# Performance work log

Hardware: AMD Instinct MI355X
Metric: run time of the kernel (lower is better)

The kernel has to match this reference:

```python
import jax, jax.numpy as jnp
import numpy as np

N_NODES = 500000
N_EDGES = 8000000
IN_DIM = 128
H1, H2, OUT = 32, 16, 2


def gcn_conv(x, W, b, src, dst, n):
    # PyG GCNConv: linear transform, add self-loops, symmetric norm, scatter-add, +bias
    x = x @ W                                   # [N, out]
    loop = jnp.arange(n, dtype=src.dtype)
    s = jnp.concatenate([src, loop])            # [E+N]
    d = jnp.concatenate([dst, loop])            # [E+N]
    deg = jax.ops.segment_sum(jnp.ones_like(d, dtype=x.dtype), d, num_segments=n)
    dinv = jnp.where(deg > 0, jax.lax.rsqrt(deg), 0.0)
    norm = dinv[s] * dinv[d]                    # [E+N]
    msg = x[s] * norm[:, None]                  # [E+N, out] gather
    out = jax.ops.segment_sum(msg, d, num_segments=n)  # scatter-add
    return out + b


def setup_inputs() -> dict:
    key = jax.random.key(0)
    ks = jax.random.split(key, 8)
    x = jax.random.normal(ks[0], (N_NODES, IN_DIM), dtype=jnp.float32)
    edge_index = jax.random.randint(ks[1], (2, N_EDGES), 0, N_NODES, dtype=jnp.int64)
    def glorot(k, fan_in, fan_out):
        lim = float(np.sqrt(6.0 / (fan_in + fan_out)))
        return jax.random.uniform(k, (fan_in, fan_out), jnp.float32, -lim, lim)
    return {
        "x": x,
        "edge_index": edge_index,
        "W1": glorot(ks[2], IN_DIM, H1),
        "b1": jnp.zeros((H1,), jnp.float32),
        "W2": glorot(ks[3], H1, H2),
        "b2": jnp.zeros((H2,), jnp.float32),
        "Wfc": glorot(ks[4], H2, OUT),
        "bfc": jnp.zeros((OUT,), jnp.float32),
    }


def reference(x, edge_index, W1, b1, W2, b2, Wfc, bfc):
    src, dst = edge_index[0], edge_index[1]
    h = jax.nn.relu(gcn_conv(x, W1, b1, src, dst, x.shape[0]))
    h = jax.nn.relu(gcn_conv(h, W2, b2, src, dst, x.shape[0]))
    logits = h @ Wfc + bfc
    return jax.nn.log_softmax(logits, axis=1)
```

## Files before the change

kernel.cpp:

```cpp
#include <hip/hip_runtime.h>

#define N_NODES 500000
#define N_EDGES 8000000
#define IN_DIM 128
#define H1 32
#define H2 16
#define NFINE 1954
#define NCOARSE 62
#define CAPA 200
#define CAPB 340

static __device__ __forceinline__ float bf2f(unsigned short u) {
    return __uint_as_float(((unsigned int)u) << 16);
}
static __device__ __forceinline__ unsigned short f2bf(float f) {
    unsigned int u = __float_as_uint(f);
    unsigned int r = (u + 0x7fffu + ((u >> 16) & 1u)) >> 16;
    return (unsigned short)r;
}
static __device__ __forceinline__ unsigned pack2bf(float a, float b) {
    return (unsigned)f2bf(a) | ((unsigned)f2bf(b) << 16);
}
static __device__ __forceinline__ float ldf(const void* p, int i, bool isf32) {
    return isf32 ? ((const float*)p)[i] : bf2f(((const unsigned short*)p)[i]);
}

__global__ __launch_bounds__(64) void k_sniff(const unsigned int* __restrict__ x,
                                              int* __restrict__ flag) {
    int bad = 0;
    for (int i = threadIdx.x; i < 1024; i += 64) {
        float v = __uint_as_float((x[i] & 0xffffu) << 16);
        if (!(fabsf(v) < 1e6f)) bad = 1;
    }
    unsigned long long m = __ballot(bad);
    if (threadIdx.x == 0) *flag = (m != 0ull) ? 1 : 0;
}

__global__ __launch_bounds__(256) void k_bhist(const int* __restrict__ dst,
                                               int* __restrict__ fhist) {
    __shared__ int h[2048];
    int tid = threadIdx.x;
    for (int i = tid; i < 2048; i += 256) h[i] = 0;
    __syncthreads();
    int i = blockIdx.x * 256 + tid;
    int stride = gridDim.x * 256;
    for (int e = i; e < N_EDGES; e += stride) {
        unsigned d = (unsigned)dst[e];
        if (d < N_NODES) atomicAdd(&h[d >> 8], 1);
    }
    __syncthreads();
    for (int i2 = tid; i2 < 2048; i2 += 256)
        if (h[i2]) atomicAdd(&fhist[i2], h[i2]);
}

__global__ __launch_bounds__(256) void k_scanf(const int* __restrict__ fhist,
                                               int* __restrict__ fbase,
                                               int* __restrict__ bcur,
                                               int* __restrict__ acur) {
    __shared__ int tmp[256];
    __shared__ int s_run;
    int tid = threadIdx.x;
    if (tid == 0) s_run = 0;
    __syncthreads();
    for (int base = 0; base < 2048; base += 256) {
        int i = base + tid;
        int v = (i < NFINE) ? fhist[i] : 0;
        int val = v;
        tmp[tid] = val;
        __syncthreads();
        for (int o = 1; o < 256; o <<= 1) {
            int t = (tid >= o) ? tmp[tid - o] : 0;
            __syncthreads();
            val += t;
            tmp[tid] = val;
            __syncthreads();
        }
        int run = s_run;
        if (i < NFINE) {
            int ex = run + val - v;
            fbase[i] = ex;
            bcur[i] = ex;
            if ((i & 31) == 0) acur[i >> 5] = ex;
        }
        __syncthreads();
        if (tid == 255) s_run = run + val;
        __syncthreads();
    }
    if (tid == 0) fbase[NFINE] = s_run;
}

__global__ __launch_bounds__(256) void k_scatA(const int* __restrict__ src,
                                               const int* __restrict__ dst,
                                               int* __restrict__ acur,
                                               unsigned* __restrict__ ebufA) {
    __shared__ unsigned stage[NCOARSE * CAPA];
    __shared__ int lcnt[NCOARSE], nn[NCOARSE], soff[NCOARSE], sbase[NCOARSE];
    __shared__ int stot;
    int tid = threadIdx.x;
    int cb = blockIdx.x * 8192;
    if (tid < NCOARSE) lcnt[tid] = 0;
    __syncthreads();
    for (int i = 0; i < 32; ++i) {
        int e = cb + (i << 8) + tid;
        if (e < N_EDGES) {
            unsigned d = (unsigned)dst[e], s = (unsigned)src[e];
            if (d < N_NODES) {
                unsigned b = d >> 13;
                unsigned p = ((d & 8191u) << 19) | s;
                int pos = atomicAdd(&lcnt[b], 1);
                if (pos < CAPA) stage[b * CAPA + pos] = p;
                else { int slot = atomicAdd(&acur[b], 1); ebufA[slot] = p; }
            }
        }
    }
    __syncthreads();
    if (tid < NCOARSE) nn[tid] = min(lcnt[tid], CAPA);
    __syncthreads();
    if (tid == 0) {
        int r = 0;
        for (int b = 0; b < NCOARSE; ++b) { soff[b] = r; r += nn[b]; }
        stot = r;
    }
    __syncthreads();
    if (tid < NCOARSE && nn[tid] > 0) sbase[tid] = atomicAdd(&acur[tid], nn[tid]);
    __syncthreads();
    for (int i = tid; i < stot; i += 256) {
        int lo = 0, hi = NCOARSE - 1;
        while (lo < hi) { int mid = (lo + hi + 1) >> 1; if (soff[mid] <= i) lo = mid; else hi = mid - 1; }
        int r = i - soff[lo];
        ebufA[sbase[lo] + r] = stage[lo * CAPA + r];
    }
}

__global__ __launch_bounds__(256) void k_scatB(const unsigned* __restrict__ ebufA,
                                               const int* __restrict__ fbase,
                                               int* __restrict__ bcur,
                                               unsigned* __restrict__ ebufB) {
    __shared__ unsigned stage[32 * CAPB];
    __shared__ int lcnt[32], nn[32], soff[32], sbase[32];
    __shared__ int stot;
    int tid = threadIdx.x;
    int a = blockIdx.x >> 3, sub = blockIdx.x & 7;
    int f0 = a * 32;
    int lb = min(32, NFINE - f0);
    int abase = fbase[f0];
    int aend = fbase[min(f0 + 32, NFINE)];
    for (int cb = abase + sub * 8192; cb < aend; cb += 8 * 8192) {
        if (tid < 32) lcnt[tid] = 0;
        __syncthreads();
        for (int i = 0; i < 32; ++i) {
            int e = cb + (i << 8) + tid;
            if (e < aend) {
                unsigned p = ebufA[e];
                unsigned dl13 = p >> 19;
                unsigned s = p & 0x7FFFFu;
                unsigned j = dl13 >> 8;
                unsigned q = ((dl13 & 255u) << 19) | s;
                int pos = atomicAdd(&lcnt[j], 1);
                if (pos < CAPB) stage[j * CAPB + pos] = q;
                else { int slot = atomicAdd(&bcur[f0 + j], 1); ebufB[slot] = q; }
            }
        }
        __syncthreads();
        if (tid < 32) nn[tid] = (tid < lb) ? min(lcnt[tid], CAPB) : 0;
        __syncthreads();
        if (tid == 0) {
            int r = 0;
            for (int b = 0; b < 32; ++b) { soff[b] = r; r += nn[b]; }
            stot = r;
        }
        __syncthreads();
        if (tid < 32 && nn[tid] > 0) sbase[tid] = atomicAdd(&bcur[f0 + tid], nn[tid]);
        __syncthreads();
        for (int i = tid; i < stot; i += 256) {
            int lo = 0, hi = 31;
            while (lo < hi) { int mid = (lo + hi + 1) >> 1; if (soff[mid] <= i) lo = mid; else hi = mid - 1; }
            int r = i - soff[lo];
            ebufB[sbase[lo] + r] = stage[lo * CAPB + r];
        }
        __syncthreads();
    }
}

__global__ __launch_bounds__(256) void k_csr(const unsigned* __restrict__ ebufB,
                                             const int* __restrict__ fbase,
                                             int* __restrict__ csr,
                                             int* __restrict__ off,
                                             float* __restrict__ dinv) {
    __shared__ int cnt[256], ctmp[256], ccur[256];
    int tid = threadIdx.x;
    int b = blockIdx.x;
    int base = fbase[b];
    int n = fbase[b + 1] - base;
    cnt[tid] = 0;
    __syncthreads();
    for (int i = tid; i < n; i += 256) {
        unsigned dl = ebufB[base + i] >> 19;
        atomicAdd(&cnt[dl], 1);
    }
    __syncthreads();
    int v = cnt[tid];
    int val = v;
    ctmp[tid] = val;
    __syncthreads();
    for (int o = 1; o < 256; o <<= 1) {
        int t = (tid >= o) ? ctmp[tid - o] : 0;
        __syncthreads();
        val += t;
        ctmp[tid] = val;
        __syncthreads();
    }
    int excl = val - v;
    off[b * 256 + tid] = base + excl;
    ccur[tid] = excl;
    dinv[b * 256 + tid] = rsqrtf((float)v + 1.0f);
    __syncthreads();
    for (int i = tid; i < n; i += 256) {
        unsigned p = ebufB[base + i];
        unsigned dl = p >> 19;
        int slot = atomicAdd(&ccur[dl], 1);
        csr[base + slot] = (int)(p & 0x7FFFFu);
    }
}

__global__ __launch_bounds__(256) void k_gemm1(const void* __restrict__ x,
                                               const void* __restrict__ w1,
                                               const float* __restrict__ dinv,
                                               unsigned* __restrict__ y1b,
                                               const int* __restrict__ flag) {
    __shared__ float wlds[IN_DIM * H1];
    const bool isf32 = (*flag != 0);
    for (int i = threadIdx.x; i < IN_DIM * H1; i += 256) wlds[i] = ldf(w1, i, isf32);
    __syncthreads();
    int node = blockIdx.x * 256 + threadIdx.x;
    if (node >= N_NODES) return;
    float acc[H1];
#pragma unroll
    for (int j = 0; j < H1; ++j) acc[j] = 0.f;
    if (isf32) {
        const float4* xr = reinterpret_cast<const float4*>((const float*)x + (size_t)node * IN_DIM);
#pragma unroll
        for (int kk = 0; kk < IN_DIM / 4; ++kk) {
            float4 v = xr[kk];
            float xe[4] = {v.x, v.y, v.z, v.w};
#pragma unroll
            for (int p = 0; p < 4; ++p) {
                const float* wr = &wlds[(kk * 4 + p) * H1];
#pragma unroll
                for (int j = 0; j < H1; ++j) acc[j] += xe[p] * wr[j];
            }
        }
    } else {
        const uint4* xr = reinterpret_cast<const uint4*>((const unsigned short*)x + (size_t)node * IN_DIM);
#pragma unroll
        for (int kk = 0; kk < IN_DIM / 8; ++kk) {
            uint4 xv = xr[kk];
            unsigned uu[4] = {xv.x, xv.y, xv.z, xv.w};
#pragma unroll
            for (int p = 0; p < 4; ++p) {
                float xlo = __uint_as_float(uu[p] << 16);
                float xhi = __uint_as_float(uu[p] & 0xffff0000u);
                const float* w0 = &wlds[(kk * 8 + p * 2) * H1];
                const float* w1r = w0 + H1;
#pragma unroll
                for (int j = 0; j < H1; ++j) acc[j] += xlo * w0[j];
#pragma unroll
                for (int j = 0; j < H1; ++j) acc[j] += xhi * w1r[j];
            }
        }
    }
    float s = dinv[node];
    unsigned o[16];
#pragma unroll
    for (int q = 0; q < 16; ++q) o[q] = pack2bf(acc[2*q] * s, acc[2*q+1] * s);
    uint4* op = reinterpret_cast<uint4*>(y1b + (size_t)node * 16);
#pragma unroll
    for (int r = 0; r < 4; ++r) op[r] = make_uint4(o[4*r], o[4*r+1], o[4*r+2], o[4*r+3]);
}

__global__ __launch_bounds__(256) void k_pull1(const int* __restrict__ off,
                                               const int* __restrict__ csr,
                                               const unsigned* __restrict__ y1b,
                                               const float* __restrict__ dinv,
                                               const void* __restrict__ b1,
                                               const void* __restrict__ w2,
                                               unsigned* __restrict__ y2b,
                                               const int* __restrict__ flag) {
    __shared__ float w2l[H1 * H2];
    __shared__ float b1l[H1];
    __shared__ float hbuf[512];
    const bool isf32 = (*flag != 0);
    int tid = threadIdx.x;
    for (int i = tid; i < H1 * H2; i += 256) w2l[i] = ldf(w2, i, isf32);
    if (tid < H1) b1l[tid] = ldf(b1, tid, isf32);
    __syncthreads();

    const int r = tid & 15;
    const int node = blockIdx.x * 16 + (tid >> 4);

    float a0 = 0.f, a1 = 0.f;
    const int beg = off[node], end = off[node + 1];
    int j = beg;
    for (; j + 4 <= end; j += 4) {
        int s0 = csr[j], s1 = csr[j + 1], s2 = csr[j + 2], s3 = csr[j + 3];
        unsigned u0 = y1b[(size_t)s0 * 16 + r];
        unsigned u1 = y1b[(size_t)s1 * 16 + r];
        unsigned u2 = y1b[(size_t)s2 * 16 + r];
        unsigned u3 = y1b[(size_t)s3 * 16 + r];
        a0 += __uint_as_float(u0 << 16) + __uint_as_float(u1 << 16)
            + __uint_as_float(u2 << 16) + __uint_as_float(u3 << 16);
        a1 += __uint_as_float(u0 & 0xffff0000u) + __uint_as_float(u1 & 0xffff0000u)
            + __uint_as_float(u2 & 0xffff0000u) + __uint_as_float(u3 & 0xffff0000u);
    }
    for (; j < end; ++j) {
        unsigned u = y1b[(size_t)csr[j] * 16 + r];
        a0 += __uint_as_float(u << 16);
        a1 += __uint_as_float(u & 0xffff0000u);
    }
    float sc = dinv[node];
    unsigned su = y1b[(size_t)node * 16 + r];
    a0 += __uint_as_float(su << 16);
    a1 += __uint_as_float(su & 0xffff0000u);
    float h0 = sc * a0 + b1l[2 * r];
    float h1 = sc * a1 + b1l[2 * r + 1];
    h0 = h0 > 0.f ? h0 : 0.f;
    h1 = h1 > 0.f ? h1 : 0.f;
    hbuf[tid * 2] = h0;
    hbuf[tid * 2 + 1] = h1;
    const float* hr = &hbuf[(tid & ~15) * 2];
    float a2 = 0.f;
#pragma unroll
    for (int k = 0; k < H1; ++k) a2 += hr[k] * w2l[k * H2 + r];
    a2 *= sc;
    int gwb = (tid & 63) & ~15;
    float v0 = __shfl(a2, (gwb + 2 * r) & 63, 64);
    float v1 = __shfl(a2, (gwb + 2 * r + 1) & 63, 64);
    if (r < 8) y2b[(size_t)node * 8 + r] = pack2bf(v0, v1);
}

__global__ __launch_bounds__(256) void k_pull2(const int* __restrict__ off,
                                               const int* __restrict__ csr,
                                               const unsigned* __restrict__ y2b,
                                               const float* __restrict__ dinv,
                                               const void* __restrict__ b2,
                                               const void* __restrict__ wfc,
                                               const void* __restrict__ bfc,
                                               void* __restrict__ out,
                                               const int* __restrict__ flag) {
    __shared__ float wl[H2 * 2];
    __shared__ float b2l[H2];
    __shared__ float bfl[2];
    const bool isf32 = (*flag != 0);
    int tid = threadIdx.x;
    if (tid < H2 * 2) wl[tid] = ldf(wfc, tid, isf32);
    if (tid < H2) b2l[tid] = ldf(b2, tid, isf32);
    if (tid < 2) bfl[tid] = ldf(bfc, tid, isf32);
    __syncthreads();

    const int r = tid & 7;
    const int node = blockIdx.x * 32 + (tid >> 3);

    float a0 = 0.f, a1 = 0.f;
    const int beg = off[node], end = off[node + 1];
    int j = beg;
    for (; j + 4 <= end; j += 4) {
        int s0 = csr[j], s1 = csr[j + 1], s2 = csr[j + 2], s3 = csr[j + 3];
        unsigned u0 = y2b[(size_t)s0 * 8 + r];
        unsigned u1 = y2b[(size_t)s1 * 8 + r];
        unsigned u2 = y2b[(size_t)s2 * 8 + r];
        unsigned u3 = y2b[(size_t)s3 * 8 + r];
        a0 += __uint_as_float(u0 << 16) + __uint_as_float(u1 << 16)
            + __uint_as_float(u2 << 16) + __uint_as_float(u3 << 16);
        a1 += __uint_as_float(u0 & 0xffff0000u) + __uint_as_float(u1 & 0xffff0000u)
            + __uint_as_float(u2 & 0xffff0000u) + __uint_as_float(u3 & 0xffff0000u);
    }
    for (; j < end; ++j) {
        unsigned u = y2b[(size_t)csr[j] * 8 + r];
        a0 += __uint_as_float(u << 16);
        a1 += __uint_as_float(u & 0xffff0000u);
    }
    float sc = dinv[node];
    unsigned su = y2b[(size_t)node * 8 + r];
    a0 += __uint_as_float(su << 16);
    a1 += __uint_as_float(su & 0xffff0000u);
    float h0 = sc * a0 + b2l[2 * r];
    float h1 = sc * a1 + b2l[2 * r + 1];
    h0 = h0 > 0.f ? h0 : 0.f;
    h1 = h1 > 0.f ? h1 : 0.f;
    float l0 = h0 * wl[4 * r]     + h1 * wl[4 * r + 2];
    float l1 = h0 * wl[4 * r + 1] + h1 * wl[4 * r + 3];
#pragma unroll
    for (int o = 4; o >= 1; o >>= 1) {
        l0 += __shfl_xor(l0, o, 8);
        l1 += __shfl_xor(l1, o, 8);
    }
    if (r == 0) {
        l0 += bfl[0];
        l1 += bfl[1];
        float mx = fmaxf(l0, l1);
        float lse = mx + logf(__expf(l0 - mx) + __expf(l1 - mx));
        if (isf32) {
            reinterpret_cast<float2*>(out)[node] = make_float2(l0 - lse, l1 - lse);
        } else {
            reinterpret_cast<unsigned*>(out)[node] =
                (unsigned)f2bf(l0 - lse) | ((unsigned)f2bf(l1 - lse) << 16);
        }
    }
}

extern "C" void kernel_launch(void* const* d_in, const int* in_sizes, int n_in,
                              void* d_out, int out_size, void* d_ws, size_t ws_size,
                              hipStream_t stream) {
    const void* x   = d_in[0];
    const int*  ei  = (const int*)d_in[1];
    const void* w1  = d_in[2];
    const void* b1  = d_in[3];
    const void* w2  = d_in[4];
    const void* b2  = d_in[5];
    const void* wfc = d_in[6];
    const void* bfc = d_in[7];
    const int* src = ei;
    const int* dst = ei + N_EDGES;

    float*    ws    = (float*)d_ws;
    int*      flag  = (int*)ws;
    float*    dinv  = ws + 64;
    int*      fhist = (int*)(ws + 500288);
    int*      fbase = (int*)(ws + 502336);
    int*      acur  = (int*)(ws + 504384);
    int*      bcur  = (int*)(ws + 504448);
    int*      off   = (int*)(ws + 506496);
    unsigned* ebufA = (unsigned*)(ws + 1006784);
    int*      csr   = (int*)(ws + 1006784);
    unsigned* ebufB = (unsigned*)(ws + 9006784);
    unsigned* y1b   = (unsigned*)(ws + 17006784);
    unsigned* y2b   = (unsigned*)(ws + 25010368);

    k_sniff<<<1, 64, 0, stream>>>((const unsigned int*)x, flag);
    hipMemsetAsync(fhist, 0, 2048 * sizeof(int), stream);
    k_bhist<<<256, 256, 0, stream>>>(dst, fhist);
    k_scanf<<<1, 256, 0, stream>>>(fhist, fbase, bcur, acur);
    k_scatA<<<977, 256, 0, stream>>>(src, dst, acur, ebufA);
    k_scatB<<<NCOARSE * 8, 256, 0, stream>>>(ebufA, fbase, bcur, ebufB);
    k_csr<<<NFINE, 256, 0, stream>>>(ebufB, fbase, csr, off, dinv);
    k_gemm1<<<NFINE, 256, 0, stream>>>(x, w1, dinv, y1b, flag);
    k_pull1<<<31250, 256, 0, stream>>>(off, csr, y1b, dinv, b1, w2, y2b, flag);
    k_pull2<<<15625, 256, 0, stream>>>(off, csr, y2b, dinv, b2, wfc, bfc, d_out, flag);
}
```

Before: 1.023 ms.

## Replace two-level bucket sort CSR build with single-pass coarse bucketing plus global-atomic fill

The CSR build drops the second LDS-staged scatter pass (scatB) and the per-fine-bucket CSR kernel. It now bins edges into 245 coarse buckets of 2048 destinations, counts per-node degree with global atomics, scans per bucket, and fills the CSR with global atomic cursors. This removes one full pass over the 8M edges and the ebufB buffer. In exchange it adds global atomic contention, a 2 MB memset, and a CSR whose order within each node is nondeterministic.

```diff
diff --git a/kernel.cpp b/kernel.cpp
--- a/kernel.cpp
+++ b/kernel.cpp
@@ -6,9 +6,8 @@
 #define H1 32
 #define H2 16
 #define NFINE 1954
-#define NCOARSE 62
-#define CAPA 200
-#define CAPB 340
+#define NC 245
+#define CAPA 64
 
 static __device__ __forceinline__ float bf2f(unsigned short u) {
     return __uint_as_float(((unsigned int)u) << 16);
@@ -37,76 +36,63 @@
 }
 
 __global__ __launch_bounds__(256) void k_bhist(const int* __restrict__ dst,
-                                               int* __restrict__ fhist) {
-    __shared__ int h[2048];
-    int tid = threadIdx.x;
-    for (int i = tid; i < 2048; i += 256) h[i] = 0;
+                                               int* __restrict__ chist) {
+    __shared__ int h[256];
+    int tid = threadIdx.x;
+    h[tid] = 0;
     __syncthreads();
     int i = blockIdx.x * 256 + tid;
     int stride = gridDim.x * 256;
     for (int e = i; e < N_EDGES; e += stride) {
         unsigned d = (unsigned)dst[e];
-        if (d < N_NODES) atomicAdd(&h[d >> 8], 1);
-    }
-    __syncthreads();
-    for (int i2 = tid; i2 < 2048; i2 += 256)
-        if (h[i2]) atomicAdd(&fhist[i2], h[i2]);
-}
-
-__global__ __launch_bounds__(256) void k_scanf(const int* __restrict__ fhist,
+        if (d < N_NODES) atomicAdd(&h[d >> 11], 1);
+    }
+    __syncthreads();
+    if (h[tid]) atomicAdd(&chist[tid], h[tid]);
+}
+
+__global__ __launch_bounds__(256) void k_scanc(const int* __restrict__ chist,
                                                int* __restrict__ fbase,
-                                               int* __restrict__ bcur,
                                                int* __restrict__ acur) {
     __shared__ int tmp[256];
-    __shared__ int s_run;
-    int tid = threadIdx.x;
-    if (tid == 0) s_run = 0;
-    __syncthreads();
-    for (int base = 0; base < 2048; base += 256) {
-        int i = base + tid;
-        int v = (i < NFINE) ? fhist[i] : 0;
-        int val = v;
+    int tid = threadIdx.x;
+    int v = (tid < NC) ? chist[tid] : 0;
+    int val = v;
+    tmp[tid] = val;
+    __syncthreads();
+    for (int o = 1; o < 256; o <<= 1) {
+        int t = (tid >= o) ? tmp[tid - o] : 0;
+        __syncthreads();
+        val += t;
         tmp[tid] = val;
         __syncthreads();
-        for (int o = 1; o < 256; o <<= 1) {
-            int t = (tid >= o) ? tmp[tid - o] : 0;
-            __syncthreads();
-            val += t;
-            tmp[tid] = val;
-            __syncthreads();
-        }
-        int run = s_run;
-        if (i < NFINE) {
-            int ex = run + val - v;
-            fbase[i] = ex;
-            bcur[i] = ex;
-            if ((i & 31) == 0) acur[i >> 5] = ex;
-        }
-        __syncthreads();
-        if (tid == 255) s_run = run + val;
-        __syncthreads();
-    }
-    if (tid == 0) fbase[NFINE] = s_run;
+    }
+    if (tid < NC) {
+        int ex = val - v;
+        fbase[tid] = ex;
+        acur[tid] = ex;
+    }
+    if (tid == NC - 1) fbase[NC] = val;
 }
 
 __global__ __launch_bounds__(256) void k_scatA(const int* __restrict__ src,
                                                const int* __restrict__ dst,
                                                int* __restrict__ acur,
                                                unsigned* __restrict__ ebufA) {
-    __shared__ unsigned stage[NCOARSE * CAPA];
-    __shared__ int lcnt[NCOARSE], nn[NCOARSE], soff[NCOARSE], sbase[NCOARSE];
+    __shared__ unsigned stage[NC * CAPA];
+    __shared__ int lcnt[NC], nn[NC], soff[NC], sbase[NC];
     __shared__ int stot;
     int tid = threadIdx.x;
     int cb = blockIdx.x * 8192;
-    if (tid < NCOARSE) lcnt[tid] = 0;
+    for (int i = tid; i < NC; i += 256) lcnt[i] = 0;
     __syncthreads();
     for (int i = 0; i < 32; ++i) {
         int e = cb + (i << 8) + tid;
         if (e < N_EDGES) {
             unsigned d = (unsigned)dst[e], s = (unsigned)src[e];
             if (d < N_NODES) {
-                unsigned b = d >> 13;
-                unsigned p = ((d & 8191u) << 19) | s;
+                unsigned b = d >> 11;
+                unsigned p = ((d & 2047u) << 19) | s;
                 int pos = atomicAdd(&lcnt[b], 1);
                 if (pos < CAPA) stage[b * CAPA + pos] = p;
                 else { int slot = atomicAdd(&acur[b], 1); ebufA[slot] = p; }
@@ -114,112 +100,88 @@
         }
     }
     __syncthreads();
-    if (tid < NCOARSE) nn[tid] = min(lcnt[tid], CAPA);
+    for (int i = tid; i < NC; i += 256) nn[i] = min(lcnt[i], CAPA);
     __syncthreads();
     if (tid == 0) {
         int r = 0;
-        for (int b = 0; b < NCOARSE; ++b) { soff[b] = r; r += nn[b]; }
+        for (int b = 0; b < NC; ++b) { soff[b] = r; r += nn[b]; }
         stot = r;
     }
     __syncthreads();
-    if (tid < NCOARSE && nn[tid] > 0) sbase[tid] = atomicAdd(&acur[tid], nn[tid]);
+    if (tid < NC && nn[tid] > 0) sbase[tid] = atomicAdd(&acur[tid], nn[tid]);
     __syncthreads();
     for (int i = tid; i < stot; i += 256) {
-        int lo = 0, hi = NCOARSE - 1;
+        int lo = 0, hi = NC - 1;
         while (lo < hi) { int mid = (lo + hi + 1) >> 1; if (soff[mid] <= i) lo = mid; else hi = mid - 1; }
         int r = i - soff[lo];
         ebufA[sbase[lo] + r] = stage[lo * CAPA + r];
     }
 }
 
-__global__ __launch_bounds__(256) void k_scatB(const unsigned* __restrict__ ebufA,
+__global__ __launch_bounds__(256) void k_cntL2(const unsigned* __restrict__ ebufA,
                                                const int* __restrict__ fbase,
-                                               int* __restrict__ bcur,
-                                               unsigned* __restrict__ ebufB) {
-    __shared__ unsigned stage[32 * CAPB];
-    __shared__ int lcnt[32], nn[32], soff[32], sbase[32];
-    __shared__ int stot;
-    int tid = threadIdx.x;
-    int a = blockIdx.x >> 3, sub = blockIdx.x & 7;
-    int f0 = a * 32;
-    int lb = min(32, NFINE - f0);
-    int abase = fbase[f0];
-    int aend = fbase[min(f0 + 32, NFINE)];
-    for (int cb = abase + sub * 8192; cb < aend; cb += 8 * 8192) {
-        if (tid < 32) lcnt[tid] = 0;
-        __syncthreads();
-        for (int i = 0; i < 32; ++i) {
-            int e = cb + (i << 8) + tid;
-            if (e < aend) {
-                unsigned p = ebufA[e];
-                unsigned dl13 = p >> 19;
-                unsigned s = p & 0x7FFFFu;
-                unsigned j = dl13 >> 8;
-                unsigned q = ((dl13 & 255u) << 19) | s;
-                int pos = atomicAdd(&lcnt[j], 1);
-                if (pos < CAPB) stage[j * CAPB + pos] = q;
-                else { int slot = atomicAdd(&bcur[f0 + j], 1); ebufB[slot] = q; }
-            }
-        }
-        __syncthreads();
-        if (tid < 32) nn[tid] = (tid < lb) ? min(lcnt[tid], CAPB) : 0;
-        __syncthreads();
-        if (tid == 0) {
-            int r = 0;
-            for (int b = 0; b < 32; ++b) { soff[b] = r; r += nn[b]; }
-            stot = r;
-        }
-        __syncthreads();
-        if (tid < 32 && nn[tid] > 0) sbase[tid] = atomicAdd(&bcur[f0 + tid], nn[tid]);
-        __syncthreads();
-        for (int i = tid; i < stot; i += 256) {
-            int lo = 0, hi = 31;
-            while (lo < hi) { int mid = (lo + hi + 1) >> 1; if (soff[mid] <= i) lo = mid; else hi = mid - 1; }
-            int r = i - soff[lo];
-            ebufB[sbase[lo] + r] = stage[lo * CAPB + r];
-        }
-        __syncthreads();
-    }
-}
-
-__global__ __launch_bounds__(256) void k_csr(const unsigned* __restrict__ ebufB,
-                                             const int* __restrict__ fbase,
-                                             int* __restrict__ csr,
-                                             int* __restrict__ off,
-                                             float* __restrict__ dinv) {
-    __shared__ int cnt[256], ctmp[256], ccur[256];
-    int tid = threadIdx.x;
-    int b = blockIdx.x;
-    int base = fbase[b];
-    int n = fbase[b + 1] - base;
-    cnt[tid] = 0;
-    __syncthreads();
-    for (int i = tid; i < n; i += 256) {
-        unsigned dl = ebufB[base + i] >> 19;
-        atomicAdd(&cnt[dl], 1);
-    }
-    __syncthreads();
-    int v = cnt[tid];
-    int val = v;
-    ctmp[tid] = val;
-    __syncthreads();
+                                               int* __restrict__ cnt) {
+    int c = blockIdx.x >> 2, q = blockIdx.x & 3;
+    int beg = fbase[c], end = fbase[c + 1];
+    int len = end - beg;
+    int qb = beg + (int)((long long)len * q >> 2);
+    int qe = beg + (int)((long long)len * (q + 1) >> 2);
+    for (int i = qb + threadIdx.x; i < qe; i += 256) {
+        unsigned p = ebufA[i];
+        int d = (c << 11) + (int)(p >> 19);
+        atomicAdd(&cnt[d], 1);
+    }
+}
+
+__global__ __launch_bounds__(256) void k_scanb(const int* __restrict__ cnt,
+                                               const int* __restrict__ fbase,
+                                               int* __restrict__ off,
+                                               int* __restrict__ cur,
+                                               float* __restrict__ dinv) {
+    __shared__ int sums[256];
+    int tid = threadIdx.x;
+    int c = blockIdx.x;
+    int nb = c << 11;
+    int v[8];
+    int loc = 0;
+#pragma unroll
+    for (int k = 0; k < 8; ++k) { v[k] = cnt[nb + tid * 8 + k]; loc += v[k]; }
+    sums[tid] = loc;
+    __syncthreads();
+    int val = loc;
     for (int o = 1; o < 256; o <<= 1) {
-        int t = (tid >= o) ? ctmp[tid - o] : 0;
+        int t = (tid >= o) ? sums[tid - o] : 0;
         __syncthreads();
         val += t;
-        ctmp[tid] = val;
+        sums[tid] = val;
         __syncthreads();
     }
-    int excl = val - v;
-    off[b * 256 + tid] = base + excl;
-    ccur[tid] = excl;
-    dinv[b * 256 + tid] = rsqrtf((float)v + 1.0f);
-    __syncthreads();
-    for (int i = tid; i < n; i += 256) {
-        unsigned p = ebufB[base + i];
-        unsigned dl = p >> 19;
-        int slot = atomicAdd(&ccur[dl], 1);
-        csr[base + slot] = (int)(p & 0x7FFFFu);
+    int run = fbase[c] + val - loc;
+#pragma unroll
+    for (int k = 0; k < 8; ++k) {
+        int d = nb + tid * 8 + k;
+        off[d] = run;
+        cur[d] = run;
+        dinv[d] = rsqrtf((float)v[k] + 1.0f);
+        run += v[k];
+    }
+    if (c == NC - 1 && tid == 255) off[NC * 2048] = run;
+}
+
+__global__ __launch_bounds__(256) void k_fill2(const unsigned* __restrict__ ebufA,
+                                               const int* __restrict__ fbase,
+                                               int* __restrict__ cur,
+                                               int* __restrict__ csr) {
+    int c = blockIdx.x >> 2, q = blockIdx.x & 3;
+    int beg = fbase[c], end = fbase[c + 1];
+    int len = end - beg;
+    int qb = beg + (int)((long long)len * q >> 2);
+    int qe = beg + (int)((long long)len * (q + 1) >> 2);
+    for (int i = qb + threadIdx.x; i < qe; i += 256) {
+        unsigned p = ebufA[i];
+        int d = (c << 11) + (int)(p >> 19);
+        int slot = atomicAdd(&cur[d], 1);
+        csr[slot] = (int)(p & 0x7FFFFu);
     }
 }
 
@@ -424,25 +386,27 @@
 
     float*    ws    = (float*)d_ws;
     int*      flag  = (int*)ws;
-    float*    dinv  = ws + 64;
-    int*      fhist = (int*)(ws + 500288);
-    int*      fbase = (int*)(ws + 502336);
-    int*      acur  = (int*)(ws + 504384);
-    int*      bcur  = (int*)(ws + 504448);
-    int*      off   = (int*)(ws + 506496);
-    unsigned* ebufA = (unsigned*)(ws + 1006784);
-    int*      csr   = (int*)(ws + 1006784);
-    unsigned* ebufB = (unsigned*)(ws + 9006784);
-    unsigned* y1b   = (unsigned*)(ws + 17006784);
-    unsigned* y2b   = (unsigned*)(ws + 25010368);
+    int*      chist = (int*)(ws + 64);
+    int*      fbase = (int*)(ws + 320);
+    int*      acur  = (int*)(ws + 576);
+    float*    dinv  = ws + 832;
+    int*      cnt   = (int*)(ws + 502592);
+    int*      off   = (int*)(ws + 1004352);
+    int*      cur   = (int*)(ws + 1506176);
+    unsigned* ebufA = (unsigned*)(ws + 2007936);
+    int*      csr   = (int*)(ws + 10007936);
+    unsigned* y1b   = (unsigned*)(ws + 18007936);
+    unsigned* y2b   = (unsigned*)(ws + 26011520);
 
     k_sniff<<<1, 64, 0, stream>>>((const unsigned int*)x, flag);
-    hipMemsetAsync(fhist, 0, 2048 * sizeof(int), stream);
-    k_bhist<<<256, 256, 0, stream>>>(dst, fhist);
-    k_scanf<<<1, 256, 0, stream>>>(fhist, fbase, bcur, acur);
+    hipMemsetAsync(chist, 0, 256 * sizeof(int), stream);
+    hipMemsetAsync(cnt, 0, (size_t)501760 * sizeof(int), stream);
+    k_bhist<<<256, 256, 0, stream>>>(dst, chist);
+    k_scanc<<<1, 256, 0, stream>>>(chist, fbase, acur);
     k_scatA<<<977, 256, 0, stream>>>(src, dst, acur, ebufA);
-    k_scatB<<<NCOARSE * 8, 256, 0, stream>>>(ebufA, fbase, bcur, ebufB);
-    k_csr<<<NFINE, 256, 0, stream>>>(ebufB, fbase, csr, off, dinv);
+    k_cntL2<<<NC * 4, 256, 0, stream>>>(ebufA, fbase, cnt);
+    k_scanb<<<NC, 256, 0, stream>>>(cnt, fbase, off, cur, dinv);
+    k_fill2<<<NC * 4, 256, 0, stream>>>(ebufA, fbase, cur, csr);
     k_gemm1<<<NFINE, 256, 0, stream>>>(x, w1, dinv, y1b, flag);
     k_pull1<<<31250, 256, 0, stream>>>(off, csr, y1b, dinv, b1, w2, y2b, flag);
     k_pull2<<<15625, 256, 0, stream>>>(off, csr, y2b, dinv, b2, wfc, bfc, d_out, flag);
```

Result: slower. 1.934 ms (+89.0%).
